# Kernel tuning notes

Hardware: AMD Instinct MI355X
Metric: run time of the kernel (lower is better)

Reference implementation:

```python
import jax, jax.numpy as jnp
import numpy as np

N, T, D, H = 128, 64, 1024, 1024
DA = 4  # hard-coded 4x4 attention grid


def setup_inputs() -> dict:
    key = jax.random.key(0)
    ks = jax.random.split(key, 6)
    x = jax.random.normal(ks[0], (N, T, D), dtype=jnp.float32)
    A = jax.random.normal(ks[1], (N, H, DA, DA), dtype=jnp.float32)
    Wx = jax.random.normal(ks[2], (D, 4 * H), dtype=jnp.float32) / np.sqrt(D)
    Wh = jax.random.normal(ks[3], (H, 4 * H), dtype=jnp.float32) / np.sqrt(H)
    Wattn = jax.random.normal(ks[4], (H, 4 * H), dtype=jnp.float32) / np.sqrt(H)
    b = jnp.zeros((4 * H,), dtype=jnp.float32)
    return {"x": x, "A": A, "Wx": Wx, "Wh": Wh, "Wattn": Wattn, "b": b}


def reference(x, A, Wx, Wh, Wattn, b):
    n, h_dim, da, _ = A.shape
    Af = A.reshape(n, h_dim, da * da)          # (N, H, P) with P = 16
    h0 = A.mean(axis=(2, 3))                   # global image feature init
    c0 = h0
    scale = jnp.sqrt(jnp.asarray(h_dim, x.dtype))

    def step(carry, xt):
        h, c = carry
        # scaled dot-product attention over P=16 spatial positions
        scores = jnp.einsum('nh,nhp->np', h, Af) / scale   # (N, P)
        w = jax.nn.softmax(scores, axis=1)
        attn = jnp.einsum('nhp,np->nh', Af, w)             # (N, H)
        # fused LSTM gates
        act = xt @ Wx + h @ Wh + attn @ Wattn + b          # (N, 4H)
        i, f, o, g = jnp.split(act, 4, axis=1)
        i = jax.nn.sigmoid(i)
        f = jax.nn.sigmoid(f)
        o = jax.nn.sigmoid(o)
        g = jnp.tanh(g)
        c_next = f * c + i * g
        h_next = o * jnp.tanh(c_next)
        return (h_next, c_next), h_next

    _, hs = jax.lax.scan(step, (h0, c0), jnp.swapaxes(x, 0, 1))  # (T, N, H)
    return jnp.swapaxes(hs, 0, 1)                                # (N, T, H)
```

## Files before the change

### kernel.cpp

```cpp
#include <hip/hip_runtime.h>
#include <hip/hip_bf16.h>
#include <cmath>

#define N_   128
#define T_   64
#define D_   1024
#define H_   1024
#define G4_  4096

typedef short bf16x8 __attribute__((ext_vector_type(8)));
typedef float f32x4  __attribute__((ext_vector_type(4)));

__device__ __forceinline__ unsigned short f2bf(float f) {
    union { float f; unsigned int u; } v; v.f = f;
    unsigned int r = (v.u + 0x7FFFu + ((v.u >> 16) & 1u)) >> 16;
    return (unsigned short)r;
}
__device__ __forceinline__ float bf2f(unsigned short s) {
    union { unsigned int u; float f; } v; v.u = ((unsigned int)s) << 16;
    return v.f;
}



__global__ void k_pack_w(const float* __restrict__ src, unsigned short* __restrict__ dst,
                         int kcoff, int kctot) {
    __shared__ float ld[64][33];
    int j0 = blockIdx.x * 32, k0 = blockIdx.y * 64;
    int tid = threadIdx.x;
    int c = tid & 31, r = tid >> 5;
    #pragma unroll
    for (int i = 0; i < 8; i++)
        ld[r + i * 8][c] = src[(long)(k0 + r + i * 8) * G4_ + j0 + c];
    __syncthreads();
    int j = tid & 31, ku = tid >> 5;
    int kcl = ku >> 2, kg = ku & 3;
    int jti = (j0 + j) >> 4, cl = (j0 + j) & 15;
    int kc = kcoff + (k0 >> 5) + kcl;
    unsigned short q[8];
    #pragma unroll
    for (int e = 0; e < 8; e++) q[e] = f2bf(ld[ku * 8 + e][j]);
    *(uint4*)(dst + ((long)(jti * kctot + kc) * 64 + kg * 16 + cl) * 8) = *(uint4*)q;
}

__global__ void k_pack_x2(const float* __restrict__ x, unsigned short* __restrict__ xP) {
    long gid = (long)blockIdx.x * 256 + threadIdx.x;
    int m = (int)(gid >> 7), u = (int)(gid & 127);
    const float* src = x + (long)m * 1024 + u * 8;
    int n = m >> 6, t = m & 63;
    int tile = t * 8 + (n >> 4);
    int kc = u >> 2, kg = u & 3, cl = n & 15;
    float4 a = *(const float4*)src, b = *(const float4*)(src + 4);
    unsigned short q[8] = {f2bf(a.x), f2bf(a.y), f2bf(a.z), f2bf(a.w),
                           f2bf(b.x), f2bf(b.y), f2bf(b.z), f2bf(b.w)};
    *(uint4*)(xP + ((long)(tile * 32 + kc) * 64 + kg * 16 + cl) * 8) = *(uint4*)q;
}

__global__ void k_pack_af(const float* __restrict__ A, unsigned short* __restrict__ AfP,
                          unsigned short* __restrict__ Af2) {
    __shared__ float ld[64][17];
    int n = blockIdx.x, h0 = blockIdx.y * 64;
    int tid = threadIdx.x;
    int hh = tid >> 2, pq = tid & 3;
    float4 v = *(const float4*)(A + ((long)n * H_ + h0 + hh) * 16 + pq * 4);
    unsigned short o[4] = {f2bf(v.x), f2bf(v.y), f2bf(v.z), f2bf(v.w)};
    *(uint2*)(Af2 + ((long)n * H_ + h0 + hh) * 16 + pq * 4) = *(uint2*)o;
    ld[hh][pq * 4 + 0] = v.x; ld[hh][pq * 4 + 1] = v.y;
    ld[hh][pq * 4 + 2] = v.z; ld[hh][pq * 4 + 3] = v.w;
    __syncthreads();
    if (tid < 128) {
        int p = tid >> 3, ku = tid & 7;
        int kc = (h0 >> 5) + (ku >> 2), kg = ku & 3;
        unsigned short q[8];
        #pragma unroll
        for (int e = 0; e < 8; e++) q[e] = f2bf(ld[ku * 8 + e][p]);
        *(uint4*)(AfP + ((long)(n * 32 + kc) * 64 + kg * 16 + p) * 8) = *(uint4*)q;
    }
}

__global__ void k_h0(const float* __restrict__ A, float* __restrict__ h,
                     float* __restrict__ c, unsigned short* __restrict__ hP0) {
    long id = (long)blockIdx.x * 256 + threadIdx.x;
    const float4* ap = (const float4*)(A + id * 16);
    float s = 0.f;
    #pragma unroll
    for (int q = 0; q < 4; q++) { float4 v = ap[q]; s += v.x + v.y + v.z + v.w; }
    float m = s * (1.0f / 16.0f);
    h[id] = m; c[id] = m;
    int n = (int)(id >> 10), j = (int)(id & 1023);
    hP0[((long)((n >> 4) * 32 + (j >> 5)) * 64 + ((j >> 3) & 3) * 16 + (n & 15)) * 8 + (j & 7)] = f2bf(m);
}

__global__ __launch_bounds__(512)
void k_part0(const float* __restrict__ hbuf, const unsigned short* __restrict__ Af2,
             float* __restrict__ partial0) {
    int n = blockIdx.x;
    int tid = threadIdx.x;
    int jh = tid * 2;
    float sp[16];
    #pragma unroll
    for (int p = 0; p < 16; p++) sp[p] = 0.f;
    #pragma unroll
    for (int u = 0; u < 2; u++) {
        float hv = hbuf[(long)n * H_ + jh + u];
        const unsigned short* afp = Af2 + ((long)n * H_ + jh + u) * 16;
        bf16x8 a0 = *(const bf16x8*)(afp);
        bf16x8 a1 = *(const bf16x8*)(afp + 8);
        #pragma unroll
        for (int p = 0; p < 8; p++) { sp[p] += hv * bf2f((unsigned short)a0[p]);
                                      sp[8+p] += hv * bf2f((unsigned short)a1[p]); }
    }
    #pragma unroll
    for (int off = 1; off < 8; off <<= 1) {
        #pragma unroll
        for (int p = 0; p < 16; p++) sp[p] += __shfl_xor(sp[p], off);
    }
    int jt = tid >> 3;
    if ((tid & 7) == 0) {
        #pragma unroll
        for (int p = 0; p < 16; p++)
            partial0[((long)n * 16 + p) * 64 + jt] = sp[p];
    }
}

__global__ __launch_bounds__(64)
void k_score_tiny(const float* __restrict__ partial, float* __restrict__ wbuf) {
    int n = blockIdx.x;
    int lane = threadIdx.x;
    int p = lane & 15, c4 = lane >> 4;
    const float* src = partial + ((long)n * 16 + p) * 64 + c4 * 16;
    float s = 0.f;
    #pragma unroll
    for (int q = 0; q < 16; q++) s += src[q];
    s += __shfl_xor(s, 16);
    s += __shfl_xor(s, 32);
    s *= (1.0f / 32.0f);
    float m = s;
    #pragma unroll
    for (int off = 1; off < 16; off <<= 1) m = fmaxf(m, __shfl_xor(m, off));
    float e = expf(s - m);
    float sum = e;
    #pragma unroll
    for (int off = 1; off < 16; off <<= 1) sum += __shfl_xor(sum, off);
    if (c4 == 0) wbuf[n * 16 + p] = e / sum;
}

__global__ __launch_bounds__(256, 2)
void k_aw(const unsigned short* __restrict__ AfP, const unsigned short* __restrict__ WattnP,
          unsigned short* __restrict__ AW) {
    int tid = threadIdx.x;
    int wv = tid >> 6, lane = tid & 63;
    int wr = wv >> 1, wc = wv & 1;
    int cl = lane & 15, kg = lane >> 4;
    int jt0 = blockIdx.x * 8 + wc * 4;
    int at0 = blockIdx.y * 8 + wr * 4;

    f32x4 acc[4][4];
    #pragma unroll
    for (int i = 0; i < 4; i++)
        #pragma unroll
        for (int j = 0; j < 4; j++) acc[i][j] = (f32x4){0.f, 0.f, 0.f, 0.f};

    const unsigned short* apx[4];
    const unsigned short* bpx[4];
    #pragma unroll
    for (int i = 0; i < 4; i++) {
        apx[i] = AfP    + (long)(at0 + i) * (32 * 512) + lane * 8;
        bpx[i] = WattnP + (long)(jt0 + i) * (32 * 512) + lane * 8;
    }
    #pragma unroll 2
    for (int kc = 0; kc < 32; kc++) {
        bf16x8 a[4], b[4];
        #pragma unroll
        for (int i = 0; i < 4; i++) a[i] = *(const bf16x8*)(apx[i] + kc * 512);
        #pragma unroll
        for (int i = 0; i < 4; i++) b[i] = *(const bf16x8*)(bpx[i] + kc * 512);
        #pragma unroll
        for (int i = 0; i < 4; i++)
            #pragma unroll
            for (int j = 0; j < 4; j++)
                acc[i][j] = __builtin_amdgcn_mfma_f32_16x16x32_bf16(a[i], b[j], acc[i][j], 0, 0, 0);
    }
    #pragma unroll
    for (int i = 0; i < 4; i++) {
        int n = at0 + i;
        #pragma unroll
        for (int j = 0; j < 4; j++) {
            int jj = (jt0 + j) * 16 + cl;
            #pragma unroll
            for (int v = 0; v < 4; v++) {
                int p = kg * 4 + v;
                AW[((long)n * G4_ + jj) * 16 + p] = f2bf(acc[i][j][v]);
            }
        }
    }
}

__global__ __launch_bounds__(256, 2)
void k_actx(const unsigned short* __restrict__ xP, const unsigned short* __restrict__ WxP,
            unsigned short* __restrict__ actx) {
    int tid = threadIdx.x;
    int wv = tid >> 6, lane = tid & 63;
    int wr = wv >> 1, wc = wv & 1;
    int cl = lane & 15, kg = lane >> 4;
    int jt0 = blockIdx.x * 8 + wc * 4;
    int at0 = blockIdx.y * 8 + wr * 4;

    f32x4 acc[4][4];
    #pragma unroll
    for (int i = 0; i < 4; i++)
        #pragma unroll
        for (int j = 0; j < 4; j++) acc[i][j] = (f32x4){0.f, 0.f, 0.f, 0.f};

    const unsigned short* apx[4];
    const unsigned short* bpx[4];
    #pragma unroll
    for (int i = 0; i < 4; i++) {
        apx[i] = xP  + (long)(at0 + i) * (32 * 512) + lane * 8;
        bpx[i] = WxP + (long)(jt0 + i) * (32 * 512) + lane * 8;
    }
    #pragma unroll 2
    for (int kc = 0; kc < 32; kc++) {
        bf16x8 a[4], b[4];
        #pragma unroll
        for (int i = 0; i < 4; i++) a[i] = *(const bf16x8*)(apx[i] + kc * 512);
        #pragma unroll
        for (int i = 0; i < 4; i++) b[i] = *(const bf16x8*)(bpx[i] + kc * 512);
        #pragma unroll
        for (int i = 0; i < 4; i++)
            #pragma unroll
            for (int j = 0; j < 4; j++)
                acc[i][j] = __builtin_amdgcn_mfma_f32_16x16x32_bf16(a[i], b[j], acc[i][j], 0, 0, 0);
    }
    #pragma unroll
    for (int i = 0; i < 4; i++) {
        long mrow = (long)(at0 + i) * 16;
        #pragma unroll
        for (int j = 0; j < 4; j++) {
            int jj = (jt0 + j) * 16 + cl;
            #pragma unroll
            for (int v = 0; v < 4; v++)
                actx[(mrow + kg * 4 + v) * G4_ + jj] = f2bf(acc[i][j][v]);
        }
    }
}


__global__ __launch_bounds__(512, 2)
void k_step(const unsigned short* __restrict__ actx,
            const unsigned short* __restrict__ hPin,
            unsigned short* __restrict__ hPout,
            const unsigned short* __restrict__ WhP,
            const unsigned short* __restrict__ AW,
            const unsigned short* __restrict__ Af2,
            const float* __restrict__ wbuf,
            const float* __restrict__ bvec,
            float* __restrict__ c,
            float* __restrict__ partOUT,
            float* __restrict__ out, int t) {
    int tid = threadIdx.x;
    int wv = tid >> 6, lane = tid & 63;
    int ks = wv & 3, rh = wv >> 2;
    int cl = lane & 15, kg = lane >> 4;
    int jt = blockIdx.x;
    int nt2 = blockIdx.y;
    int colbase = jt * 16;

    f32x4 acc[4];
    #pragma unroll
    for (int g = 0; g < 4; g++) acc[g] = (f32x4){0.f, 0.f, 0.f, 0.f};

    const unsigned short* abase = hPin + ((long)(nt2 * 2 + rh) * 32 + ks * 8) * 512 + lane * 8;
    const unsigned short* bb[4];
    #pragma unroll
    for (int g = 0; g < 4; g++)
        bb[g] = WhP + ((long)(g * 64 + jt) * 32 + ks * 8) * 512 + lane * 8;

    #pragma unroll
    for (int i = 0; i < 8; i++) {
        bf16x8 a = *(const bf16x8*)(abase + i * 512);
        #pragma unroll
        for (int g = 0; g < 4; g++) {
            bf16x8 b = *(const bf16x8*)(bb[g] + i * 512);
            acc[g] = __builtin_amdgcn_mfma_f32_16x16x32_bf16(a, b, acc[g], 0, 0, 0);
        }
    }

    __shared__ float red[3][2][64][17];
    __shared__ float act[4][32][17];
    if (ks != 0) {
        #pragma unroll
        for (int g = 0; g < 4; g++)
            #pragma unroll
            for (int v = 0; v < 4; v++) red[ks - 1][rh][lane][g * 4 + v] = acc[g][v];
    }
    __syncthreads();
    if (ks == 0) {
        #pragma unroll
        for (int g = 0; g < 4; g++)
            #pragma unroll
            for (int v = 0; v < 4; v++) {
                float s = acc[g][v] + red[0][rh][lane][g*4+v] + red[1][rh][lane][g*4+v]
                        + red[2][rh][lane][g*4+v];
                act[g][rh * 16 + kg * 4 + v][cl] = s;
            }
    }
    __syncthreads();

    int nloc = tid >> 4, jl = tid & 15;
    int n = nt2 * 32 + nloc, jh = colbase + jl;
    float wv16[16];
    #pragma unroll
    for (int p = 0; p < 16; p++) wv16[p] = wbuf[n * 16 + p];

    long rm = (long)(t * 8 + (n >> 4)) * 16 + (n & 15);
    float s4[4];
    #pragma unroll
    for (int g = 0; g < 4; g++) {
        int j = g * 1024 + jh;
        const unsigned short* awp = AW + ((long)n * G4_ + j) * 16;
        bf16x8 aw0 = *(const bf16x8*)(awp);
        bf16x8 aw1 = *(const bf16x8*)(awp + 8);
        float at = 0.f;
        #pragma unroll
        for (int p = 0; p < 8; p++) at += wv16[p]     * bf2f((unsigned short)aw0[p]);
        #pragma unroll
        for (int p = 0; p < 8; p++) at += wv16[8 + p] * bf2f((unsigned short)aw1[p]);
        s4[g] = act[g][nloc][jl] + bf2f(actx[rm * G4_ + j]) + at + bvec[j];
    }
    float ig = 1.f / (1.f + expf(-s4[0]));
    float fg = 1.f / (1.f + expf(-s4[1]));
    float og = 1.f / (1.f + expf(-s4[2]));
    float gg = tanhf(s4[3]);
    long idx = (long)n * H_ + jh;
    float cn = fg * c[idx] + ig * gg;
    float hn = og * tanhf(cn);
    c[idx] = cn;
    out[((long)n * T_ + t) * H_ + jh] = hn;
    hPout[((long)((n >> 4) * 32 + (jh >> 5)) * 64 + ((jh >> 3) & 3) * 16 + (n & 15)) * 8 + (jh & 7)] = f2bf(hn);

    const unsigned short* afp = Af2 + ((long)n * H_ + jh) * 16;
    bf16x8 af0 = *(const bf16x8*)(afp);
    bf16x8 af1 = *(const bf16x8*)(afp + 8);
    float sp[16];
    #pragma unroll
    for (int p = 0; p < 8; p++) { sp[p]     = hn * bf2f((unsigned short)af0[p]);
                                  sp[8 + p] = hn * bf2f((unsigned short)af1[p]); }
    #pragma unroll
    for (int off = 1; off < 16; off <<= 1) {
        #pragma unroll
        for (int p = 0; p < 16; p++) sp[p] += __shfl_xor(sp[p], off);
    }
    float outv = 0.f;
    #pragma unroll
    for (int p = 0; p < 16; p++) if (jl == p) outv = sp[p];
    partOUT[((long)n * 16 + jl) * 64 + jt] = outv;
}


extern "C" void kernel_launch(void* const* d_in, const int* in_sizes, int n_in,
                              void* d_out, int out_size, void* d_ws, size_t ws_size,
                              hipStream_t stream) {
    const float* x     = (const float*)d_in[0];
    const float* A     = (const float*)d_in[1];
    const float* Wx    = (const float*)d_in[2];
    const float* Wh    = (const float*)d_in[3];
    const float* Wattn = (const float*)d_in[4];
    const float* b     = (const float*)d_in[5];
    float* out = (float*)d_out;

    char* ws = (char*)d_ws;
    size_t off = 0;
    auto alloc = [&](size_t bytes) -> void* {
        void* p = ws + off;
        off += (bytes + 255) & ~(size_t)255;
        return p;
    };
    unsigned short* xP     = (unsigned short*)alloc((size_t)512 * 32 * 512 * 2);
    unsigned short* WxP    = (unsigned short*)alloc((size_t)256 * 32 * 512 * 2);
    unsigned short* WhP    = (unsigned short*)alloc((size_t)256 * 32 * 512 * 2);
    unsigned short* WattnP = (unsigned short*)alloc((size_t)256 * 32 * 512 * 2);
    unsigned short* AfP    = (unsigned short*)alloc((size_t)128 * 32 * 512 * 2);
    unsigned short* Af2    = (unsigned short*)alloc((size_t)N_ * H_ * 16 * 2);
    unsigned short* AW     = (unsigned short*)alloc((size_t)N_ * G4_ * 16 * 2);
    unsigned short* actx   = (unsigned short*)alloc((size_t)8192 * G4_ * 2);
    float*          hbuf   = (float*)alloc((size_t)N_ * H_ * 4);
    float*          cbuf   = (float*)alloc((size_t)N_ * H_ * 4);
    unsigned short* hP0    = (unsigned short*)alloc((size_t)8 * 32 * 512 * 2);
    unsigned short* hP1    = (unsigned short*)alloc((size_t)8 * 32 * 512 * 2);
    float*          part0  = (float*)alloc((size_t)N_ * 16 * 64 * 4);
    float*          part1  = (float*)alloc((size_t)N_ * 16 * 64 * 4);
    float*          wbuf   = (float*)alloc((size_t)N_ * 16 * 4);

    k_pack_w<<<dim3(128, 16), dim3(256), 0, stream>>>(Wx,    WxP,    0, 32);
    k_pack_w<<<dim3(128, 16), dim3(256), 0, stream>>>(Wh,    WhP,    0, 32);
    k_pack_w<<<dim3(128, 16), dim3(256), 0, stream>>>(Wattn, WattnP, 0, 32);
    k_pack_x2<<<dim3(4096), dim3(256), 0, stream>>>(x, xP);
    k_pack_af<<<dim3(128, 16), dim3(256), 0, stream>>>(A, AfP, Af2);
    k_h0<<<dim3(512), dim3(256), 0, stream>>>(A, hbuf, cbuf, hP0);
    k_part0<<<dim3(N_), dim3(512), 0, stream>>>(hbuf, Af2, part0);
    k_aw<<<dim3(32, 16), dim3(256), 0, stream>>>(AfP, WattnP, AW);
    k_actx<<<dim3(32, 64), dim3(256), 0, stream>>>(xP, WxP, actx);

    for (int t = 0; t < T_; t++) {
        unsigned short* hin  = (t & 1) ? hP1 : hP0;
        unsigned short* hout = (t & 1) ? hP0 : hP1;
        float* pIN  = (t & 1) ? part1 : part0;
        float* pOUT = (t & 1) ? part0 : part1;
        k_score_tiny<<<dim3(N_), dim3(64), 0, stream>>>(pIN, wbuf);
        k_step<<<dim3(64, 4), dim3(512), 0, stream>>>(actx, hin, hout, WhP, AW, Af2,
                                                      wbuf, b, cbuf, pOUT, out, t);
    }
}
```

Baseline: 1.061 ms.

## Switch precompute GEMMs to 32x32x16 MFMA with new 32-row packed layouts

The x@Wx and Af@Wattn precompute GEMMs now use 32x32x16 bf16 MFMA instructions instead of 16x16x32, with new packing kernels for the 32-row operand layout. The block grid is transposed so blockIdx.x walks the M tiles. Each wave still covers a 64x64 output tile, but with fewer, larger MFMAs, which aims to raise matrix-core throughput and cut operand-load overhead. The epilogue stores are remapped to the 32x32 accumulator layout. These GEMMs run once before the 64-step recurrent loop, so any gain is limited to that one-time part of the total time.

```diff
diff --git a/kernel.cpp b/kernel.cpp
--- a/kernel.cpp
+++ b/kernel.cpp
@@ -8,8 +8,9 @@
 #define H_   1024
 #define G4_  4096
 
-typedef short bf16x8 __attribute__((ext_vector_type(8)));
-typedef float f32x4  __attribute__((ext_vector_type(4)));
+typedef short bf16x8  __attribute__((ext_vector_type(8)));
+typedef float f32x4   __attribute__((ext_vector_type(4)));
+typedef float f32x16  __attribute__((ext_vector_type(16)));
 
 __device__ __forceinline__ unsigned short f2bf(float f) {
     union { float f; unsigned int u; } v; v.f = f;
@@ -43,21 +44,39 @@
     *(uint4*)(dst + ((long)(jti * kctot + kc) * 64 + kg * 16 + cl) * 8) = *(uint4*)q;
 }
 
-__global__ void k_pack_x2(const float* __restrict__ x, unsigned short* __restrict__ xP) {
+__global__ void k_pack_w32(const float* __restrict__ src, unsigned short* __restrict__ dst) {
+    __shared__ float ld[64][33];
+    int j0 = blockIdx.x * 32, k0 = blockIdx.y * 64;
+    int tid = threadIdx.x;
+    int c = tid & 31, r = tid >> 5;
+    #pragma unroll
+    for (int i = 0; i < 8; i++)
+        ld[r + i * 8][c] = src[(long)(k0 + r + i * 8) * G4_ + j0 + c];
+    __syncthreads();
+    int cl = tid & 31, kgrp = (tid >> 5) & 1, kcl = tid >> 6;
+    int kc = (k0 >> 4) + kcl;
+    unsigned short q[8];
+    #pragma unroll
+    for (int e = 0; e < 8; e++) q[e] = f2bf(ld[kcl * 16 + kgrp * 8 + e][cl]);
+    *(uint4*)(dst + (((long)blockIdx.x * 64 + kc) * 64 + kgrp * 32 + cl) * 8) = *(uint4*)q;
+}
+
+__global__ void k_pack_x32(const float* __restrict__ x, unsigned short* __restrict__ xP32) {
     long gid = (long)blockIdx.x * 256 + threadIdx.x;
-    int m = (int)(gid >> 7), u = (int)(gid & 127);
-    const float* src = x + (long)m * 1024 + u * 8;
-    int n = m >> 6, t = m & 63;
-    int tile = t * 8 + (n >> 4);
-    int kc = u >> 2, kg = u & 3, cl = n & 15;
+    int mm = (int)(gid >> 7), u = (int)(gid & 127);
+    const float* src = x + (long)mm * 1024 + u * 8;
+    int n = mm >> 6, t = mm & 63;
+    int tile = t * 4 + (n >> 5);
+    int row = n & 31;
+    int kc = u >> 1, kgrp = u & 1;
     float4 a = *(const float4*)src, b = *(const float4*)(src + 4);
     unsigned short q[8] = {f2bf(a.x), f2bf(a.y), f2bf(a.z), f2bf(a.w),
                            f2bf(b.x), f2bf(b.y), f2bf(b.z), f2bf(b.w)};
-    *(uint4*)(xP + ((long)(tile * 32 + kc) * 64 + kg * 16 + cl) * 8) = *(uint4*)q;
-}
-
-__global__ void k_pack_af(const float* __restrict__ A, unsigned short* __restrict__ AfP,
-                          unsigned short* __restrict__ Af2) {
+    *(uint4*)(xP32 + (((long)tile * 64 + kc) * 64 + kgrp * 32 + row) * 8) = *(uint4*)q;
+}
+
+__global__ void k_pack_af32(const float* __restrict__ A, unsigned short* __restrict__ AfP32,
+                            unsigned short* __restrict__ Af2) {
     __shared__ float ld[64][17];
     int n = blockIdx.x, h0 = blockIdx.y * 64;
     int tid = threadIdx.x;
@@ -70,11 +89,12 @@
     __syncthreads();
     if (tid < 128) {
         int p = tid >> 3, ku = tid & 7;
-        int kc = (h0 >> 5) + (ku >> 2), kg = ku & 3;
+        int kc = (h0 >> 4) + (ku >> 1), kgrp = ku & 1;
+        int row = (n & 1) * 16 + p;
         unsigned short q[8];
         #pragma unroll
         for (int e = 0; e < 8; e++) q[e] = f2bf(ld[ku * 8 + e][p]);
-        *(uint4*)(AfP + ((long)(n * 32 + kc) * 64 + kg * 16 + p) * 8) = *(uint4*)q;
+        *(uint4*)(AfP32 + (((long)(n >> 1) * 64 + kc) * 64 + kgrp * 32 + row) * 8) = *(uint4*)q;
     }
 }
 
@@ -146,101 +166,106 @@
 }
 
 __global__ __launch_bounds__(256, 2)
-void k_aw(const unsigned short* __restrict__ AfP, const unsigned short* __restrict__ WattnP,
+void k_aw(const unsigned short* __restrict__ AfP32, const unsigned short* __restrict__ WattnP32,
           unsigned short* __restrict__ AW) {
     int tid = threadIdx.x;
     int wv = tid >> 6, lane = tid & 63;
     int wr = wv >> 1, wc = wv & 1;
-    int cl = lane & 15, kg = lane >> 4;
-    int jt0 = blockIdx.x * 8 + wc * 4;
-    int at0 = blockIdx.y * 8 + wr * 4;
-
-    f32x4 acc[4][4];
-    #pragma unroll
-    for (int i = 0; i < 4; i++)
-        #pragma unroll
-        for (int j = 0; j < 4; j++) acc[i][j] = (f32x4){0.f, 0.f, 0.f, 0.f};
-
-    const unsigned short* apx[4];
-    const unsigned short* bpx[4];
-    #pragma unroll
-    for (int i = 0; i < 4; i++) {
-        apx[i] = AfP    + (long)(at0 + i) * (32 * 512) + lane * 8;
-        bpx[i] = WattnP + (long)(jt0 + i) * (32 * 512) + lane * 8;
+    int at0 = blockIdx.x * 4 + wr * 2;
+    int jt0 = blockIdx.y * 4 + wc * 2;
+
+    f32x16 acc[2][2];
+    #pragma unroll
+    for (int i = 0; i < 2; i++)
+        #pragma unroll
+        for (int j = 0; j < 2; j++)
+            #pragma unroll
+            for (int r = 0; r < 16; r++) acc[i][j][r] = 0.f;
+
+    const unsigned short* apx[2];
+    const unsigned short* bpx[2];
+    #pragma unroll
+    for (int i = 0; i < 2; i++) {
+        apx[i] = AfP32     + (long)(at0 + i) * (64 * 512) + lane * 8;
+        bpx[i] = WattnP32  + (long)(jt0 + i) * (64 * 512) + lane * 8;
     }
     #pragma unroll 2
-    for (int kc = 0; kc < 32; kc++) {
-        bf16x8 a[4], b[4];
-        #pragma unroll
-        for (int i = 0; i < 4; i++) a[i] = *(const bf16x8*)(apx[i] + kc * 512);
-        #pragma unroll
-        for (int i = 0; i < 4; i++) b[i] = *(const bf16x8*)(bpx[i] + kc * 512);
-        #pragma unroll
-        for (int i = 0; i < 4; i++)
-            #pragma unroll
-            for (int j = 0; j < 4; j++)
-                acc[i][j] = __builtin_amdgcn_mfma_f32_16x16x32_bf16(a[i], b[j], acc[i][j], 0, 0, 0);
-    }
-    #pragma unroll
-    for (int i = 0; i < 4; i++) {
-        int n = at0 + i;
-        #pragma unroll
-        for (int j = 0; j < 4; j++) {
-            int jj = (jt0 + j) * 16 + cl;
-            #pragma unroll
-            for (int v = 0; v < 4; v++) {
-                int p = kg * 4 + v;
-                AW[((long)n * G4_ + jj) * 16 + p] = f2bf(acc[i][j][v]);
+    for (int kc = 0; kc < 64; kc++) {
+        bf16x8 a[2], b[2];
+        #pragma unroll
+        for (int i = 0; i < 2; i++) a[i] = *(const bf16x8*)(apx[i] + kc * 512);
+        #pragma unroll
+        for (int i = 0; i < 2; i++) b[i] = *(const bf16x8*)(bpx[i] + kc * 512);
+        #pragma unroll
+        for (int i = 0; i < 2; i++)
+            #pragma unroll
+            for (int j = 0; j < 2; j++)
+                acc[i][j] = __builtin_amdgcn_mfma_f32_32x32x16_bf16(a[i], b[j], acc[i][j], 0, 0, 0);
+    }
+    int col_l = lane & 31, rbase = 4 * (lane >> 5);
+    #pragma unroll
+    for (int i = 0; i < 2; i++) {
+        #pragma unroll
+        for (int j = 0; j < 2; j++) {
+            int col = (jt0 + j) * 32 + col_l;
+            #pragma unroll
+            for (int r = 0; r < 16; r++) {
+                int grow = (at0 + i) * 32 + (r & 3) + 8 * (r >> 2) + rbase;
+                int n = grow >> 4, p = grow & 15;
+                AW[((long)n * G4_ + col) * 16 + p] = f2bf(acc[i][j][r]);
             }
         }
     }
 }
 
 __global__ __launch_bounds__(256, 2)
-void k_actx(const unsigned short* __restrict__ xP, const unsigned short* __restrict__ WxP,
+void k_actx(const unsigned short* __restrict__ xP32, const unsigned short* __restrict__ WxP32,
             unsigned short* __restrict__ actx) {
     int tid = threadIdx.x;
     int wv = tid >> 6, lane = tid & 63;
     int wr = wv >> 1, wc = wv & 1;
-    int cl = lane & 15, kg = lane >> 4;
-    int jt0 = blockIdx.x * 8 + wc * 4;
-    int at0 = blockIdx.y * 8 + wr * 4;
-
-    f32x4 acc[4][4];
-    #pragma unroll
-    for (int i = 0; i < 4; i++)
-        #pragma unroll
-        for (int j = 0; j < 4; j++) acc[i][j] = (f32x4){0.f, 0.f, 0.f, 0.f};
-
-    const unsigned short* apx[4];
-    const unsigned short* bpx[4];
-    #pragma unroll
-    for (int i = 0; i < 4; i++) {
-        apx[i] = xP  + (long)(at0 + i) * (32 * 512) + lane * 8;
-        bpx[i] = WxP + (long)(jt0 + i) * (32 * 512) + lane * 8;
+    int at0 = blockIdx.x * 4 + wr * 2;
+    int jt0 = blockIdx.y * 4 + wc * 2;
+
+    f32x16 acc[2][2];
+    #pragma unroll
+    for (int i = 0; i < 2; i++)
+        #pragma unroll
+        for (int j = 0; j < 2; j++)
+            #pragma unroll
+            for (int r = 0; r < 16; r++) acc[i][j][r] = 0.f;
+
+    const unsigned short* apx[2];
+    const unsigned short* bpx[2];
+    #pragma unroll
+    for (int i = 0; i < 2; i++) {
+        apx[i] = xP32  + (long)(at0 + i) * (64 * 512) + lane * 8;
+        bpx[i] = WxP32 + (long)(jt0 + i) * (64 * 512) + lane * 8;
     }
     #pragma unroll 2
-    for (int kc = 0; kc < 32; kc++) {
-        bf16x8 a[4], b[4];
-        #pragma unroll
-        for (int i = 0; i < 4; i++) a[i] = *(const bf16x8*)(apx[i] + kc * 512);
-        #pragma unroll
-        for (int i = 0; i < 4; i++) b[i] = *(const bf16x8*)(bpx[i] + kc * 512);
-        #pragma unroll
-        for (int i = 0; i < 4; i++)
-            #pragma unroll
-            for (int j = 0; j < 4; j++)
-                acc[i][j] = __builtin_amdgcn_mfma_f32_16x16x32_bf16(a[i], b[j], acc[i][j], 0, 0, 0);
-    }
-    #pragma unroll
-    for (int i = 0; i < 4; i++) {
-        long mrow = (long)(at0 + i) * 16;
-        #pragma unroll
-        for (int j = 0; j < 4; j++) {
-            int jj = (jt0 + j) * 16 + cl;
-            #pragma unroll
-            for (int v = 0; v < 4; v++)
-                actx[(mrow + kg * 4 + v) * G4_ + jj] = f2bf(acc[i][j][v]);
+    for (int kc = 0; kc < 64; kc++) {
+        bf16x8 a[2], b[2];
+        #pragma unroll
+        for (int i = 0; i < 2; i++) a[i] = *(const bf16x8*)(apx[i] + kc * 512);
+        #pragma unroll
+        for (int i = 0; i < 2; i++) b[i] = *(const bf16x8*)(bpx[i] + kc * 512);
+        #pragma unroll
+        for (int i = 0; i < 2; i++)
+            #pragma unroll
+            for (int j = 0; j < 2; j++)
+                acc[i][j] = __builtin_amdgcn_mfma_f32_32x32x16_bf16(a[i], b[j], acc[i][j], 0, 0, 0);
+    }
+    int col_l = lane & 31, rbase = 4 * (lane >> 5);
+    #pragma unroll
+    for (int i = 0; i < 2; i++) {
+        #pragma unroll
+        for (int j = 0; j < 2; j++) {
+            int col = (jt0 + j) * 32 + col_l;
+            #pragma unroll
+            for (int r = 0; r < 16; r++) {
+                long m = (long)(at0 + i) * 32 + (r & 3) + 8 * (r >> 2) + rbase;
+                actx[m * G4_ + col] = f2bf(acc[i][j][r]);
+            }
         }
     }
 }
@@ -376,11 +401,11 @@
         off += (bytes + 255) & ~(size_t)255;
         return p;
     };
-    unsigned short* xP     = (unsigned short*)alloc((size_t)512 * 32 * 512 * 2);
-    unsigned short* WxP    = (unsigned short*)alloc((size_t)256 * 32 * 512 * 2);
+    unsigned short* xP32   = (unsigned short*)alloc((size_t)256 * 64 * 512 * 2);
+    unsigned short* WxP32  = (unsigned short*)alloc((size_t)128 * 64 * 512 * 2);
     unsigned short* WhP    = (unsigned short*)alloc((size_t)256 * 32 * 512 * 2);
-    unsigned short* WattnP = (unsigned short*)alloc((size_t)256 * 32 * 512 * 2);
-    unsigned short* AfP    = (unsigned short*)alloc((size_t)128 * 32 * 512 * 2);
+    unsigned short* WatP32 = (unsigned short*)alloc((size_t)128 * 64 * 512 * 2);
+    unsigned short* AfP32  = (unsigned short*)alloc((size_t)64 * 64 * 512 * 2);
     unsigned short* Af2    = (unsigned short*)alloc((size_t)N_ * H_ * 16 * 2);
     unsigned short* AW     = (unsigned short*)alloc((size_t)N_ * G4_ * 16 * 2);
     unsigned short* actx   = (unsigned short*)alloc((size_t)8192 * G4_ * 2);
@@ -392,15 +417,15 @@
     float*          part1  = (float*)alloc((size_t)N_ * 16 * 64 * 4);
     float*          wbuf   = (float*)alloc((size_t)N_ * 16 * 4);
 
-    k_pack_w<<<dim3(128, 16), dim3(256), 0, stream>>>(Wx,    WxP,    0, 32);
-    k_pack_w<<<dim3(128, 16), dim3(256), 0, stream>>>(Wh,    WhP,    0, 32);
-    k_pack_w<<<dim3(128, 16), dim3(256), 0, stream>>>(Wattn, WattnP, 0, 32);
-    k_pack_x2<<<dim3(4096), dim3(256), 0, stream>>>(x, xP);
-    k_pack_af<<<dim3(128, 16), dim3(256), 0, stream>>>(A, AfP, Af2);
+    k_pack_w32<<<dim3(128, 16), dim3(256), 0, stream>>>(Wx,    WxP32);
+    k_pack_w  <<<dim3(128, 16), dim3(256), 0, stream>>>(Wh,    WhP, 0, 32);
+    k_pack_w32<<<dim3(128, 16), dim3(256), 0, stream>>>(Wattn, WatP32);
+    k_pack_x32<<<dim3(4096), dim3(256), 0, stream>>>(x, xP32);
+    k_pack_af32<<<dim3(128, 16), dim3(256), 0, stream>>>(A, AfP32, Af2);
     k_h0<<<dim3(512), dim3(256), 0, stream>>>(A, hbuf, cbuf, hP0);
     k_part0<<<dim3(N_), dim3(512), 0, stream>>>(hbuf, Af2, part0);
-    k_aw<<<dim3(32, 16), dim3(256), 0, stream>>>(AfP, WattnP, AW);
-    k_actx<<<dim3(32, 64), dim3(256), 0, stream>>>(xP, WxP, actx);
+    k_aw<<<dim3(16, 32), dim3(256), 0, stream>>>(AfP32, WatP32, AW);
+    k_actx<<<dim3(64, 32), dim3(256), 0, stream>>>(xP32, WxP32, actx);
 
     for (int t = 0; t < T_; t++) {
         unsigned short* hin  = (t & 1) ? hP1 : hP0;
```

Measured after the change: 1.035 ms. 1.03x faster.
